# Performance work log

Measured on AMD Instinct MI355X. Metric: run time of the kernel, lower is better.

## Reference

```python
import jax, jax.numpy as jnp
import numpy as np

KERNEL = 5  # hardcoded moving-average kernel size in the model
PAD = (KERNEL - 1) // 2


def setup_inputs() -> dict:
    key = jax.random.key(0)
    k1, k2, k3, k4, k5 = jax.random.split(key, 5)
    b, seq_len, pred_len, c = 64, 336, 720, 33 * 54
    x = jax.random.normal(k1, (b, seq_len, c), dtype=jnp.float32)
    W_seasonal = jax.random.normal(k2, (pred_len, seq_len), dtype=jnp.float32) * 0.02
    b_seasonal = jax.random.normal(k3, (pred_len,), dtype=jnp.float32) * 0.02
    W_trend = jax.random.normal(k4, (pred_len, seq_len), dtype=jnp.float32) * 0.02
    b_trend = jax.random.normal(k5, (pred_len,), dtype=jnp.float32) * 0.02
    return {"x": x, "W_seasonal": W_seasonal, "b_seasonal": b_seasonal,
            "W_trend": W_trend, "b_trend": b_trend}


def _moving_avg(x):
    # x: [b, t, c]; replicate-pad the time axis then k-window mean (stride 1)
    xp = jnp.pad(x, ((0, 0), (PAD, PAD), (0, 0)), mode="edge")
    cs = jnp.cumsum(xp, axis=1)
    cs = jnp.concatenate([jnp.zeros_like(cs[:, :1]), cs], axis=1)
    return (cs[:, KERNEL:] - cs[:, :-KERNEL]) / KERNEL  # [b, t, c]


def reference(x, W_seasonal, b_seasonal, W_trend, b_trend):
    # All 33 chunks use the same weights, so the per-chunk loop is equivalent
    # to processing the full 1782-channel tensor at once.
    trend = _moving_avg(x)            # [b, t, c]
    seasonal = x - trend              # [b, t, c]
    # torch Linear over the time axis: y[b,p,c] = sum_t x[b,t,c] * W[p,t] + bias[p]
    out = (jnp.einsum("btc,pt->bpc", seasonal, W_seasonal) + b_seasonal[None, :, None]
           + jnp.einsum("btc,pt->bpc", trend, W_trend) + b_trend[None, :, None])
    return jnp.maximum(out, 0.0)      # torch.clip(min=0)
```

## Files before the change

kernel.cpp:

```cpp
#include <hip/hip_runtime.h>
#include <hip/hip_bf16.h>
#include <stdint.h>

#define T_SEQ 336
#define NKT   11
#define P_LEN 720
#define NM16  48
#define C_LEN 1782
#define NB    64
#define CTILE 112
#define NCT   16
#define BPITCH 360

typedef __attribute__((ext_vector_type(4))) float f32x4;
typedef __attribute__((ext_vector_type(8))) short s16x8;

__device__ __forceinline__ unsigned short f2bf(float f) {
  unsigned int u = __builtin_bit_cast(unsigned int, f);
  u += 0x7FFFu + ((u >> 16) & 1u);
  return (unsigned short)(u >> 16);
}

__global__ __launch_bounds__(64) void prep_w(
    const float* __restrict__ Ws, const float* __restrict__ bs,
    const float* __restrict__ Wt, const float* __restrict__ bt,
    unsigned short* __restrict__ apack, float* __restrict__ bias) {
  const int p   = blockIdx.x;
  const int tid = threadIdx.x;
  if (tid < NKT * 4) {
    const int kt = tid >> 2;
    const int lg = tid & 3;
    const float* wsr = Ws + (size_t)p * T_SEQ;
    const float* wtr = Wt + (size_t)p * T_SEQ;
    union { s16x8 v; unsigned short u[8]; } pk;
#pragma unroll
    for (int j = 0; j < 8; ++j) {
      const int k = kt * 32 + lg * 8 + j;
      float val = 0.f;
      if (p < P_LEN && k < T_SEQ) {
        float d;
        if (k == 0) {
          d = 3.f*(wtr[0]-wsr[0]) + 2.f*(wtr[1]-wsr[1]) + (wtr[2]-wsr[2]);
        } else if (k == T_SEQ-1) {
          d = 3.f*(wtr[T_SEQ-1]-wsr[T_SEQ-1]) + 2.f*(wtr[T_SEQ-2]-wsr[T_SEQ-2])
              + (wtr[T_SEQ-3]-wsr[T_SEQ-3]);
        } else {
          int lo = (k-2 < 0) ? 0 : k-2;
          int hi = (k+2 > T_SEQ-1) ? T_SEQ-1 : k+2;
          d = 0.f;
          for (int t = lo; t <= hi; ++t) d += wtr[t]-wsr[t];
        }
        val = wsr[k] + 0.2f*d;
      }
      pk.u[j] = f2bf(val);
    }
    const int m16 = p >> 4;
    const int l16 = p & 15;
    *(s16x8*)&apack[(size_t)(((m16*NKT + kt) * 64) + lg*16 + l16) * 8] = pk.v;
  }
  if (tid == 0 && p < P_LEN) bias[p] = bs[p] + bt[p];
}

__global__ __launch_bounds__(512, 4) void gemm_kernel(
    const float* __restrict__ x, const unsigned short* __restrict__ apack,
    const float* __restrict__ bias, float* __restrict__ out) {
  __shared__ __align__(16) unsigned short Bp[CTILE * BPITCH];

  const int bid = blockIdx.x;
  const int ct  = bid & 15;
  const int b   = bid >> 4;
  const int c0  = ct * CTILE;

  const int tid  = threadIdx.x;
  const int lane = tid & 63;
  const int wid  = tid >> 6;
  const int l16  = lane & 15;
  const int lg   = lane >> 4;

  const float* xb = x + (size_t)b * T_SEQ * C_LEN;
  const s16x8* ap = (const s16x8*)apack;

  for (int i = tid; i < 42 * 56; i += 512) {
    const int cp = i % 56;
    const int kg = i / 56;
    int c = c0 + cp * 2; if (c > C_LEN - 2) c = C_LEN - 2;
    float2 v[8];
#pragma unroll
    for (int j = 0; j < 8; ++j)
      v[j] = *(const float2*)(xb + (size_t)(kg * 8 + j) * C_LEN + c);
    union { s16x8 vv; uint32_t dw[4]; } pa, pb;
#pragma unroll
    for (int h = 0; h < 4; ++h) {
      uint32_t ra, rb;
      asm("v_cvt_pk_bf16_f32 %0, %1, %2" : "=v"(ra) : "v"(v[2*h].x), "v"(v[2*h+1].x));
      asm("v_cvt_pk_bf16_f32 %0, %1, %2" : "=v"(rb) : "v"(v[2*h].y), "v"(v[2*h+1].y));
      pa.dw[h] = ra; pb.dw[h] = rb;
    }
    *(s16x8*)&Bp[(cp * 2)     * BPITCH + kg * 8] = pa.vv;
    *(s16x8*)&Bp[(cp * 2 + 1) * BPITCH + kg * 8] = pb.vv;
  }
  {
    const s16x8 z = {};
    for (int i = tid; i < CTILE * 3; i += 512)
      *(s16x8*)&Bp[(i / 3) * BPITCH + T_SEQ + (i % 3) * 8] = z;
  }
  __syncthreads();

  const size_t ob = (size_t)b * P_LEN * C_LEN;

#pragma unroll 1
  for (int mp = 0; mp < 3; ++mp) {
    const int m16a = mp * 16 + wid * 2;
    float bv[2][4];
#pragma unroll
    for (int m = 0; m < 2; ++m) {
      const int pb0 = (m16a + m) * 16 + lg * 4;
#pragma unroll
      for (int r = 0; r < 4; ++r)
        bv[m][r] = (pb0 + r < P_LEN) ? bias[pb0 + r] : 0.f;
    }

    f32x4 acc[2][7] = {};
#pragma unroll
    for (int kt = 0; kt < NKT; ++kt) {
      const s16x8 af0 = ap[(size_t)((m16a)     * NKT + kt) * 64 + lane];
      const s16x8 af1 = ap[(size_t)((m16a + 1) * NKT + kt) * 64 + lane];
      s16x8 bf[7];
#pragma unroll
      for (int n = 0; n < 7; ++n)
        bf[n] = *(const s16x8*)&Bp[(n * 16 + l16) * BPITCH + kt * 32 + lg * 8];
#pragma unroll
      for (int n = 0; n < 7; ++n) {
        acc[0][n] = __builtin_amdgcn_mfma_f32_16x16x32_bf16(
            af0, bf[n], acc[0][n], 0, 0, 0);
        acc[1][n] = __builtin_amdgcn_mfma_f32_16x16x32_bf16(
            af1, bf[n], acc[1][n], 0, 0, 0);
      }
    }

#pragma unroll
    for (int m = 0; m < 2; ++m) {
      const int m16 = m16a + m;
      if (m16 < 45) {
        const int pb0 = m16 * 16 + lg * 4;
#pragma unroll
        for (int n = 0; n < 7; ++n) {
          const int cc = c0 + n * 16 + l16;
          if (cc < C_LEN) {
#pragma unroll
            for (int r = 0; r < 4; ++r) {
              float vv = acc[m][n][r] + bv[m][r];
              out[ob + (size_t)(pb0 + r) * C_LEN + cc] = fmaxf(vv, 0.f);
            }
          }
        }
      }
    }
  }
}

extern "C" void kernel_launch(void* const* d_in, const int* in_sizes, int n_in,
                              void* d_out, int out_size, void* d_ws, size_t ws_size,
                              hipStream_t stream) {
  (void)in_sizes; (void)n_in; (void)out_size; (void)ws_size;
  const float* x  = (const float*)d_in[0];
  const float* Ws = (const float*)d_in[1];
  const float* bs = (const float*)d_in[2];
  const float* Wt = (const float*)d_in[3];
  const float* bt = (const float*)d_in[4];
  float* out = (float*)d_out;

  unsigned short* apack = (unsigned short*)d_ws;
  float* biasp = (float*)((char*)d_ws + (size_t)NM16 * NKT * 1024);

  prep_w<<<dim3(768), dim3(64), 0, stream>>>(Ws, bs, Wt, bt, apack, biasp);
  gemm_kernel<<<dim3(NB * NCT), dim3(512), 0, stream>>>(x, apack, biasp, out);
}
```

Measured before the change: 198.5 us.

## Make GEMM persistent over column panels with double-buffered LDS staging

Each block now handles 7 column panels of 64 channels instead of one 112-channel tile, with a grid of 256 blocks mapped per XCD by batch. The next panel's x slice is loaded, converted to bf16 and written to a second LDS buffer while the current panel's MFMAs run. LDS rows use an XOR swizzle to avoid bank conflicts. This is meant to hide the global load latency of x behind compute. In exchange, fewer and larger blocks run, occupancy drops (launch bounds 2), and each thread needs 48 scalar loads per stage, which raises register pressure.

After: 324.1 us. +63.3%, slower.

```diff
diff --git a/kernel.cpp b/kernel.cpp
--- a/kernel.cpp
+++ b/kernel.cpp
@@ -8,9 +8,9 @@
 #define NM16  48
 #define C_LEN 1782
 #define NB    64
-#define CTILE 112
-#define NCT   16
-#define BPITCH 360
+#define CT    64
+#define NPANEL 7
+#define SPITCH 384
 
 typedef __attribute__((ext_vector_type(4))) float f32x4;
 typedef __attribute__((ext_vector_type(8))) short s16x8;
@@ -61,15 +61,16 @@
   if (tid == 0 && p < P_LEN) bias[p] = bs[p] + bt[p];
 }
 
-__global__ __launch_bounds__(512, 4) void gemm_kernel(
+__global__ __launch_bounds__(512, 2) void gemm_kernel(
     const float* __restrict__ x, const unsigned short* __restrict__ apack,
     const float* __restrict__ bias, float* __restrict__ out) {
-  __shared__ __align__(16) unsigned short Bp[CTILE * BPITCH];
+  __shared__ __align__(16) unsigned short Bp[2][CT * SPITCH];
 
   const int bid = blockIdx.x;
-  const int ct  = bid & 15;
-  const int b   = bid >> 4;
-  const int c0  = ct * CTILE;
+  const int xcd = bid & 7;
+  const int idx = bid >> 3;
+  const int b   = xcd * 8 + (idx >> 2);
+  const int ct0 = (idx & 3) * NPANEL;
 
   const int tid  = threadIdx.x;
   const int lane = tid & 63;
@@ -80,82 +81,105 @@
   const float* xb = x + (size_t)b * T_SEQ * C_LEN;
   const s16x8* ap = (const s16x8*)apack;
 
-  for (int i = tid; i < 42 * 56; i += 512) {
-    const int cp = i % 56;
-    const int kg = i / 56;
-    int c = c0 + cp * 2; if (c > C_LEN - 2) c = C_LEN - 2;
-    float2 v[8];
-#pragma unroll
-    for (int j = 0; j < 8; ++j)
-      v[j] = *(const float2*)(xb + (size_t)(kg * 8 + j) * C_LEN + c);
-    union { s16x8 vv; uint32_t dw[4]; } pa, pb;
-#pragma unroll
-    for (int h = 0; h < 4; ++h) {
-      uint32_t ra, rb;
-      asm("v_cvt_pk_bf16_f32 %0, %1, %2" : "=v"(ra) : "v"(v[2*h].x), "v"(v[2*h+1].x));
-      asm("v_cvt_pk_bf16_f32 %0, %1, %2" : "=v"(rb) : "v"(v[2*h].y), "v"(v[2*h+1].y));
-      pa.dw[h] = ra; pb.dw[h] = rb;
-    }
-    *(s16x8*)&Bp[(cp * 2)     * BPITCH + kg * 8] = pa.vv;
-    *(s16x8*)&Bp[(cp * 2 + 1) * BPITCH + kg * 8] = pb.vv;
-  }
   {
     const s16x8 z = {};
-    for (int i = tid; i < CTILE * 3; i += 512)
-      *(s16x8*)&Bp[(i / 3) * BPITCH + T_SEQ + (i % 3) * 8] = z;
+    for (int i = tid; i < 2 * CT * 6; i += 512) {
+      const int bf = i / (CT * 6);
+      const int r  = i % (CT * 6);
+      const int c  = r / 6;
+      const int s  = 42 + r % 6;
+      *(s16x8*)&Bp[bf][c * SPITCH + ((s ^ (c & 7)) << 3)] = z;
+    }
   }
+
+  auto stage = [&](int pp) {
+    if (tid < 448) {
+      const int cl = tid & 63;
+      const int kq = tid >> 6;
+      int c = (ct0 + pp) * CT + cl;
+      if (c > C_LEN - 1) c = C_LEN - 1;
+      float f[48];
+#pragma unroll
+      for (int i = 0; i < 48; ++i)
+        f[i] = xb[(size_t)(kq * 48 + i) * C_LEN + c];
+      union { uint32_t dw[24]; s16x8 v[6]; } u;
+#pragma unroll
+      for (int h = 0; h < 24; ++h) {
+        uint32_t rr;
+        asm("v_cvt_pk_bf16_f32 %0, %1, %2"
+            : "=v"(rr) : "v"(f[2*h]), "v"(f[2*h+1]));
+        u.dw[h] = rr;
+      }
+      unsigned short* dst = &Bp[pp & 1][cl * SPITCH];
+#pragma unroll
+      for (int q = 0; q < 6; ++q)
+        *(s16x8*)(dst + (((kq * 6 + q) ^ (cl & 7)) << 3)) = u.v[q];
+    }
+  };
+
+  stage(0);
   __syncthreads();
 
   const size_t ob = (size_t)b * P_LEN * C_LEN;
 
 #pragma unroll 1
-  for (int mp = 0; mp < 3; ++mp) {
-    const int m16a = mp * 16 + wid * 2;
-    float bv[2][4];
-#pragma unroll
-    for (int m = 0; m < 2; ++m) {
-      const int pb0 = (m16a + m) * 16 + lg * 4;
-#pragma unroll
-      for (int r = 0; r < 4; ++r)
-        bv[m][r] = (pb0 + r < P_LEN) ? bias[pb0 + r] : 0.f;
-    }
-
-    f32x4 acc[2][7] = {};
-#pragma unroll
-    for (int kt = 0; kt < NKT; ++kt) {
-      const s16x8 af0 = ap[(size_t)((m16a)     * NKT + kt) * 64 + lane];
-      const s16x8 af1 = ap[(size_t)((m16a + 1) * NKT + kt) * 64 + lane];
-      s16x8 bf[7];
-#pragma unroll
-      for (int n = 0; n < 7; ++n)
-        bf[n] = *(const s16x8*)&Bp[(n * 16 + l16) * BPITCH + kt * 32 + lg * 8];
-#pragma unroll
-      for (int n = 0; n < 7; ++n) {
-        acc[0][n] = __builtin_amdgcn_mfma_f32_16x16x32_bf16(
-            af0, bf[n], acc[0][n], 0, 0, 0);
-        acc[1][n] = __builtin_amdgcn_mfma_f32_16x16x32_bf16(
-            af1, bf[n], acc[1][n], 0, 0, 0);
-      }
-    }
-
-#pragma unroll
-    for (int m = 0; m < 2; ++m) {
-      const int m16 = m16a + m;
-      if (m16 < 45) {
-        const int pb0 = m16 * 16 + lg * 4;
-#pragma unroll
-        for (int n = 0; n < 7; ++n) {
-          const int cc = c0 + n * 16 + l16;
-          if (cc < C_LEN) {
-#pragma unroll
-            for (int r = 0; r < 4; ++r) {
-              float vv = acc[m][n][r] + bv[m][r];
-              out[ob + (size_t)(pb0 + r) * C_LEN + cc] = fmaxf(vv, 0.f);
+  for (int p = 0; p < NPANEL; ++p) {
+    if (p + 1 < NPANEL) stage(p + 1);
+    const unsigned short* B = &Bp[p & 1][0];
+    const int c0 = (ct0 + p) * CT;
+
+#pragma unroll 1
+    for (int mp = 0; mp < 3; ++mp) {
+      const int m16a = mp * 16 + wid * 2;
+      float bv[2][4];
+#pragma unroll
+      for (int m = 0; m < 2; ++m) {
+        const int pb0 = (m16a + m) * 16 + lg * 4;
+#pragma unroll
+        for (int r = 0; r < 4; ++r)
+          bv[m][r] = (pb0 + r < P_LEN) ? bias[pb0 + r] : 0.f;
+      }
+
+      f32x4 acc[2][4] = {};
+#pragma unroll
+      for (int kt = 0; kt < NKT; ++kt) {
+        const s16x8 af0 = ap[(size_t)((m16a)     * NKT + kt) * 64 + lane];
+        const s16x8 af1 = ap[(size_t)((m16a + 1) * NKT + kt) * 64 + lane];
+        s16x8 bf[4];
+#pragma unroll
+        for (int n = 0; n < 4; ++n) {
+          const int c = n * 16 + l16;
+          bf[n] = *(const s16x8*)&B[c * SPITCH + ((((kt << 2) + lg) ^ (c & 7)) << 3)];
+        }
+#pragma unroll
+        for (int n = 0; n < 4; ++n) {
+          acc[0][n] = __builtin_amdgcn_mfma_f32_16x16x32_bf16(
+              af0, bf[n], acc[0][n], 0, 0, 0);
+          acc[1][n] = __builtin_amdgcn_mfma_f32_16x16x32_bf16(
+              af1, bf[n], acc[1][n], 0, 0, 0);
+        }
+      }
+
+#pragma unroll
+      for (int m = 0; m < 2; ++m) {
+        const int m16 = m16a + m;
+        if (m16 < 45) {
+          const int pb0 = m16 * 16 + lg * 4;
+#pragma unroll
+          for (int n = 0; n < 4; ++n) {
+            const int cc = c0 + n * 16 + l16;
+            if (cc < C_LEN) {
+#pragma unroll
+              for (int r = 0; r < 4; ++r) {
+                float vv = acc[m][n][r] + bv[m][r];
+                out[ob + (size_t)(pb0 + r) * C_LEN + cc] = fmaxf(vv, 0.f);
+              }
             }
           }
         }
       }
     }
+    __syncthreads();
   }
 }
 
@@ -174,5 +198,5 @@
   float* biasp = (float*)((char*)d_ws + (size_t)NM16 * NKT * 1024);
 
   prep_w<<<dim3(768), dim3(64), 0, stream>>>(Ws, bs, Wt, bt, apack, biasp);
-  gemm_kernel<<<dim3(NB * NCT), dim3(512), 0, stream>>>(x, apack, biasp, out);
-}
+  gemm_kernel<<<dim3(256), dim3(512), 0, stream>>>(x, apack, biasp, out);
+}
```
